# Optimization experiments

Measured on AMD Instinct MI355X. Metric: run time of the kernel, lower is better.

## Reference

```python
import jax, jax.numpy as jnp
import numpy as np

N_NODES = 100000
N_EDGES = 1600000
D_IN = 128
D_OUT = 128


def setup_inputs() -> dict:
    key = jax.random.key(0)
    k1, k2, k3, k4, k5 = jax.random.split(key, 5)
    h = jax.random.normal(k1, (N_NODES, D_IN), dtype=jnp.float32)
    src = jax.random.randint(k2, (N_EDGES,), 0, N_NODES, dtype=jnp.int64)
    dst = jax.random.randint(k3, (N_EDGES,), 0, N_NODES, dtype=jnp.int64)
    W = jax.random.normal(k4, (2 * D_IN, D_OUT), dtype=jnp.float32) * (1.0 / np.sqrt(2 * D_IN))
    b = jax.random.normal(k5, (D_OUT,), dtype=jnp.float32) * 0.01
    return {"h": h, "src": src, "dst": dst, "W": W, "b": b}


def reference(h, src, dst, W, b):
    # copy_u + mean: scatter-mean of source features onto destination nodes
    msg_sum = jax.ops.segment_sum(h[src], dst, num_segments=N_NODES)  # [N, D_IN]
    deg = jax.ops.segment_sum(jnp.ones((src.shape[0],), h.dtype), dst, num_segments=N_NODES)  # [N]
    h_N = jnp.where(deg[:, None] > 0, msg_sum / jnp.maximum(deg, 1.0)[:, None], 0.0)
    h_total = jnp.concatenate([h, h_N], axis=1)  # [N, 2*D_IN]
    return h_total @ W + b
```

## Files before the change

### kernel.cpp

```cpp
#include <hip/hip_runtime.h>
#include <stdint.h>

#define N_NODES 100000
#define D 128
#define BN 64
#define NB ((N_NODES + BN - 1) / BN)
#define CAPN 64
#define HPAD 136

typedef short bf16x8 __attribute__((ext_vector_type(8)));
typedef float f32x4 __attribute__((ext_vector_type(4)));

__device__ __forceinline__ unsigned short f2bf(float f) {
    unsigned int x = __float_as_uint(f);
    unsigned int r = x + 0x7fffu + ((x >> 16) & 1u);
    return (unsigned short)(r >> 16);
}
__device__ __forceinline__ float blo(unsigned int u) { return __uint_as_float(u << 16); }
__device__ __forceinline__ float bhi(unsigned int u) { return __uint_as_float(u & 0xffff0000u); }

__global__ __launch_bounds__(256) void prep_k(
    const float* __restrict__ h, unsigned short* __restrict__ h_bf,
    const float* __restrict__ W, unsigned short* __restrict__ Wf,
    const int* __restrict__ src, const int* __restrict__ dst,
    int* __restrict__ cnt, unsigned int* __restrict__ pairs,
    int n_edges, int cblocks, int epb)
{
    int bid = blockIdx.x;
    int t = threadIdx.x;

    if (bid < cblocks) {
        size_t base = ((size_t)bid * 256 + t) * 4;
        float4 v = *(const float4*)(h + base);

        for (int i = t; i < epb; i += 256) {
            int e = bid * epb + i;
            if (e < n_edges) {
                int d = dst[e];
                int slot = atomicAdd(&cnt[d], 1);
                if (slot < CAPN)
                    pairs[(size_t)d * CAPN + slot] = (unsigned int)src[e];
            }
        }

        ushort4 o;
        o.x = f2bf(v.x); o.y = f2bf(v.y); o.z = f2bf(v.z); o.w = f2bf(v.w);
        *(ushort4*)(h_bf + base) = o;
    } else {
        int gid = (bid - cblocks) * 256 + t;
        if (gid < 64 * 64) {
            int f = gid >> 6, l = gid & 63;
            int kt = f >> 3, ct = f & 7;
            int n = ct * 16 + (l & 15);
            int kb = kt * 32 + (l >> 4) * 8;
            #pragma unroll
            for (int j = 0; j < 8; ++j)
                Wf[(size_t)f * 512 + l * 8 + j] = f2bf(W[(size_t)(kb + j) * D + n]);
        }
    }
}

__global__ __launch_bounds__(512, 8) void aggemm_k(
    const unsigned short* __restrict__ h_bf, const unsigned int* __restrict__ pairs,
    const int* __restrict__ cnt_g, const unsigned short* __restrict__ Wf,
    const float* __restrict__ bias, float* __restrict__ out)
{
    __shared__ unsigned short hNs[BN][HPAD];

    int t = threadIdx.x;
    int b = blockIdx.x;
    int wv = t >> 6, l = t & 63;
    int q = l >> 4, lq = l & 15;
    int nbase = b * BN;

    #pragma unroll
    for (int p = 0; p < 2; ++p) {
        int nl = p * 32 + wv * 4 + q;
        int n = nbase + nl;
        int dg = 0;
        if (n < N_NODES) { dg = cnt_g[n]; if (dg > CAPN) dg = CAPN; }
        const unsigned int* ps = pairs + (size_t)(n < N_NODES ? n : 0) * CAPN;
        float a0 = 0.f, a1 = 0.f, a2 = 0.f, a3 = 0.f;
        float a4 = 0.f, a5 = 0.f, a6 = 0.f, a7 = 0.f;
        int i = 0;
        for (; i + 4 <= dg; i += 4) {
            uint4 s4 = *(const uint4*)(ps + i);
            uint4 u0 = *(const uint4*)(h_bf + (size_t)s4.x * D + lq * 8);
            uint4 u1 = *(const uint4*)(h_bf + (size_t)s4.y * D + lq * 8);
            uint4 u2 = *(const uint4*)(h_bf + (size_t)s4.z * D + lq * 8);
            uint4 u3 = *(const uint4*)(h_bf + (size_t)s4.w * D + lq * 8);
            a0 += (blo(u0.x) + blo(u1.x)) + (blo(u2.x) + blo(u3.x));
            a1 += (bhi(u0.x) + bhi(u1.x)) + (bhi(u2.x) + bhi(u3.x));
            a2 += (blo(u0.y) + blo(u1.y)) + (blo(u2.y) + blo(u3.y));
            a3 += (bhi(u0.y) + bhi(u1.y)) + (bhi(u2.y) + bhi(u3.y));
            a4 += (blo(u0.z) + blo(u1.z)) + (blo(u2.z) + blo(u3.z));
            a5 += (bhi(u0.z) + bhi(u1.z)) + (bhi(u2.z) + bhi(u3.z));
            a6 += (blo(u0.w) + blo(u1.w)) + (blo(u2.w) + blo(u3.w));
            a7 += (bhi(u0.w) + bhi(u1.w)) + (bhi(u2.w) + bhi(u3.w));
        }
        for (; i < dg; ++i) {
            uint4 u = *(const uint4*)(h_bf + (size_t)ps[i] * D + lq * 8);
            a0 += blo(u.x); a1 += bhi(u.x);
            a2 += blo(u.y); a3 += bhi(u.y);
            a4 += blo(u.z); a5 += bhi(u.z);
            a6 += blo(u.w); a7 += bhi(u.w);
        }
        float invd = dg > 0 ? 1.0f / (float)dg : 0.f;
        uint4 o;
        o.x = ((unsigned int)f2bf(a1 * invd) << 16) | f2bf(a0 * invd);
        o.y = ((unsigned int)f2bf(a3 * invd) << 16) | f2bf(a2 * invd);
        o.z = ((unsigned int)f2bf(a5 * invd) << 16) | f2bf(a4 * invd);
        o.w = ((unsigned int)f2bf(a7 * invd) << 16) | f2bf(a6 * invd);
        *(uint4*)(&hNs[nl][lq * 8]) = o;
    }
    __syncthreads();

    int rt = wv >> 1, ch = wv & 1;
    int lrow = l & 15, lqd = l >> 4;
    int lr = rt * 16 + lrow;
    int r0 = nbase + lr; if (r0 > N_NODES - 1) r0 = N_NODES - 1;

    f32x4 acc[4];
    #pragma unroll
    for (int c = 0; c < 4; ++c) acc[c] = (f32x4){0.f, 0.f, 0.f, 0.f};

    const unsigned short* wf_lane = Wf + l * 8;

    #pragma unroll
    for (int kt = 0; kt < 8; ++kt) {
        int ko = (kt & 3) * 32 + lqd * 8;
        bf16x8 a;
        if (kt < 4)
            a = *(const bf16x8*)(h_bf + (size_t)r0 * D + ko);
        else
            a = *(const bf16x8*)(&hNs[lr][ko]);
        #pragma unroll
        for (int c = 0; c < 4; ++c) {
            int ct = ch * 4 + c;
            bf16x8 bfr = *(const bf16x8*)(wf_lane + (size_t)(kt * 8 + ct) * 512);
            acc[c] = __builtin_amdgcn_mfma_f32_16x16x32_bf16(a, bfr, acc[c], 0, 0, 0);
        }
    }

    int col = l & 15, qd = l >> 4;
    #pragma unroll
    for (int c = 0; c < 4; ++c) {
        int ct = ch * 4 + c;
        float bv = bias[ct * 16 + col];
        #pragma unroll
        for (int r = 0; r < 4; ++r) {
            int row = nbase + rt * 16 + qd * 4 + r;
            if (row < N_NODES)
                out[(size_t)row * D + ct * 16 + col] = acc[c][r] + bv;
        }
    }
}


extern "C" void kernel_launch(void* const* d_in, const int* in_sizes, int n_in,
                              void* d_out, int out_size, void* d_ws, size_t ws_size,
                              hipStream_t stream) {
    const float* h  = (const float*)d_in[0];
    const int* src  = (const int*)d_in[1];
    const int* dst  = (const int*)d_in[2];
    const float* W  = (const float*)d_in[3];
    const float* b  = (const float*)d_in[4];
    float* out      = (float*)d_out;
    int n_edges = in_sizes[1];

    char* ws = (char*)d_ws;
    unsigned short* h_bf  = (unsigned short*)ws;
    unsigned int* pairs   = (unsigned int*)(h_bf + (size_t)N_NODES * D);
    unsigned short* Wf    = (unsigned short*)(pairs + (size_t)N_NODES * CAPN);
    int* cnt              = (int*)(Wf + 64 * 512);

    hipMemsetAsync(cnt, 0, N_NODES * sizeof(int), stream);

    int cblocks = (int)(((size_t)N_NODES * D / 4 + 255) / 256);
    int epb = (n_edges + cblocks - 1) / cblocks;
    hipLaunchKernelGGL(prep_k, dim3(cblocks + 16), dim3(256), 0, stream,
                       h, h_bf, W, Wf, src, dst, cnt, pairs, n_edges, cblocks, epb);

    hipLaunchKernelGGL(aggemm_k, dim3(NB), dim3(512), 0, stream,
                       h_bf, pairs, cnt, Wf, b, out);
}
```

Baseline: 265.1 us.

## Bucket edges per 64-node block with shared-histogram partition and in-block counting sort

Replaces per-destination global atomics and fixed 64-slot adjacency lists with a two-level partition. Each block builds a shared-memory histogram over 64-node buckets and reserves a range with one global atomic per bucket. The aggregation kernel then counting-sorts its bucket's packed (src, local dst) pairs in LDS. This removes heavy global atomic contention and the mostly empty padded adjacency storage. In exchange it adds large shared arrays per block (lowering occupancy), an extra in-block sort with several barriers, and a bucket cap of 1536 edges that could drop edges on skewed inputs.

```diff
diff --git a/kernel.cpp b/kernel.cpp
--- a/kernel.cpp
+++ b/kernel.cpp
@@ -5,7 +5,8 @@
 #define D 128
 #define BN 64
 #define NB ((N_NODES + BN - 1) / BN)
-#define CAPN 64
+#define EPB 4096
+#define CAP 1536
 #define HPAD 136
 
 typedef short bf16x8 __attribute__((ext_vector_type(8)));
@@ -24,30 +25,38 @@
     const float* __restrict__ W, unsigned short* __restrict__ Wf,
     const int* __restrict__ src, const int* __restrict__ dst,
     int* __restrict__ cnt, unsigned int* __restrict__ pairs,
-    int n_edges, int cblocks, int epb)
+    int n_edges, int partb)
 {
+    __shared__ int hist[NB];
+    __shared__ int lc[NB];
+
     int bid = blockIdx.x;
     int t = threadIdx.x;
 
-    if (bid < cblocks) {
-        size_t base = ((size_t)bid * 256 + t) * 4;
-        float4 v = *(const float4*)(h + base);
-
-        for (int i = t; i < epb; i += 256) {
-            int e = bid * epb + i;
-            if (e < n_edges) {
-                int d = dst[e];
-                int slot = atomicAdd(&cnt[d], 1);
-                if (slot < CAPN)
-                    pairs[(size_t)d * CAPN + slot] = (unsigned int)src[e];
-            }
-        }
-
-        ushort4 o;
-        o.x = f2bf(v.x); o.y = f2bf(v.y); o.z = f2bf(v.z); o.w = f2bf(v.w);
-        *(ushort4*)(h_bf + base) = o;
-    } else {
-        int gid = (bid - cblocks) * 256 + t;
+    if (bid < partb) {
+        for (int i = t; i < NB; i += 256) { hist[i] = 0; lc[i] = 0; }
+        __syncthreads();
+        int base = bid * EPB;
+        int lim = n_edges - base; if (lim > EPB) lim = EPB; if (lim < 0) lim = 0;
+        for (int i = t; i < lim; i += 256)
+            atomicAdd(&hist[dst[base + i] >> 6], 1);
+        __syncthreads();
+        for (int i = t; i < NB; i += 256) {
+            int c = hist[i];
+            hist[i] = c ? atomicAdd(&cnt[i], c) : 0;
+        }
+        __syncthreads();
+        for (int i = t; i < lim; i += 256) {
+            int e = base + i;
+            int d = dst[e], b = d >> 6;
+            int slot = atomicAdd(&lc[b], 1);
+            int off = hist[b] + slot;
+            if (off < CAP)
+                pairs[(size_t)b * CAP + off] =
+                    (unsigned int)src[e] | ((unsigned int)(d & 63) << 17);
+        }
+    } else if (bid < partb + 16) {
+        int gid = (bid - partb) * 256 + t;
         if (gid < 64 * 64) {
             int f = gid >> 6, l = gid & 63;
             int kt = f >> 3, ct = f & 7;
@@ -57,6 +66,14 @@
             for (int j = 0; j < 8; ++j)
                 Wf[(size_t)f * 512 + l * 8 + j] = f2bf(W[(size_t)(kb + j) * D + n]);
         }
+    } else {
+        size_t base = ((size_t)(bid - partb - 16) * 256 + t) * 4;
+        if (base < (size_t)N_NODES * D) {
+            float4 v = *(const float4*)(h + base);
+            ushort4 o;
+            o.x = f2bf(v.x); o.y = f2bf(v.y); o.z = f2bf(v.z); o.w = f2bf(v.w);
+            *(ushort4*)(h_bf + base) = o;
+        }
     }
 }
 
@@ -65,30 +82,70 @@
     const int* __restrict__ cnt_g, const unsigned short* __restrict__ Wf,
     const float* __restrict__ bias, float* __restrict__ out)
 {
+    __shared__ unsigned int lp[CAP];
+    __shared__ unsigned int srt[CAP];
+    __shared__ int counts[BN];
+    __shared__ int startp[BN];
+    __shared__ int cursor[BN];
     __shared__ unsigned short hNs[BN][HPAD];
 
     int t = threadIdx.x;
     int b = blockIdx.x;
     int wv = t >> 6, l = t & 63;
+    size_t e0 = (size_t)b * CAP;
+    int cnt = cnt_g[b];
+    if (cnt > CAP) cnt = CAP;
+
+    if (t < BN) counts[t] = 0;
+    __syncthreads();
+
+    for (int i = t; i < cnt; i += 512) {
+        unsigned int p = pairs[e0 + i];
+        lp[i] = p;
+        atomicAdd(&counts[p >> 17], 1);
+    }
+    __syncthreads();
+
+    if (t < BN) startp[t] = counts[t];
+    __syncthreads();
+    #pragma unroll
+    for (int off = 1; off < BN; off <<= 1) {
+        int v = 0;
+        if (t < BN && t >= off) v = startp[t - off];
+        __syncthreads();
+        if (t < BN) startp[t] += v;
+        __syncthreads();
+    }
+    if (t < BN) {
+        int ex = startp[t] - counts[t];
+        startp[t] = ex;
+        cursor[t] = ex;
+    }
+    __syncthreads();
+
+    for (int i = t; i < cnt; i += 512) {
+        unsigned int p = lp[i];
+        int s = atomicAdd(&cursor[p >> 17], 1);
+        srt[s] = p & 0x1FFFFu;
+    }
+    __syncthreads();
+
     int q = l >> 4, lq = l & 15;
     int nbase = b * BN;
-
-    #pragma unroll
-    for (int p = 0; p < 2; ++p) {
-        int nl = p * 32 + wv * 4 + q;
-        int n = nbase + nl;
-        int dg = 0;
-        if (n < N_NODES) { dg = cnt_g[n]; if (dg > CAPN) dg = CAPN; }
-        const unsigned int* ps = pairs + (size_t)(n < N_NODES ? n : 0) * CAPN;
+    #pragma unroll
+    for (int p2 = 0; p2 < 2; ++p2) {
+        int nl = p2 * 32 + wv * 4 + q;
+        int dg = counts[nl], s0 = startp[nl];
         float a0 = 0.f, a1 = 0.f, a2 = 0.f, a3 = 0.f;
         float a4 = 0.f, a5 = 0.f, a6 = 0.f, a7 = 0.f;
         int i = 0;
         for (; i + 4 <= dg; i += 4) {
-            uint4 s4 = *(const uint4*)(ps + i);
-            uint4 u0 = *(const uint4*)(h_bf + (size_t)s4.x * D + lq * 8);
-            uint4 u1 = *(const uint4*)(h_bf + (size_t)s4.y * D + lq * 8);
-            uint4 u2 = *(const uint4*)(h_bf + (size_t)s4.z * D + lq * 8);
-            uint4 u3 = *(const uint4*)(h_bf + (size_t)s4.w * D + lq * 8);
+            int s0i = srt[s0 + i],     s1i = srt[s0 + i + 1];
+            int s2i = srt[s0 + i + 2], s3i = srt[s0 + i + 3];
+            uint4 u0 = *(const uint4*)(h_bf + (size_t)s0i * D + lq * 8);
+            uint4 u1 = *(const uint4*)(h_bf + (size_t)s1i * D + lq * 8);
+            uint4 u2 = *(const uint4*)(h_bf + (size_t)s2i * D + lq * 8);
+            uint4 u3 = *(const uint4*)(h_bf + (size_t)s3i * D + lq * 8);
             a0 += (blo(u0.x) + blo(u1.x)) + (blo(u2.x) + blo(u3.x));
             a1 += (bhi(u0.x) + bhi(u1.x)) + (bhi(u2.x) + bhi(u3.x));
             a2 += (blo(u0.y) + blo(u1.y)) + (blo(u2.y) + blo(u3.y));
@@ -99,7 +156,7 @@
             a7 += (bhi(u0.w) + bhi(u1.w)) + (bhi(u2.w) + bhi(u3.w));
         }
         for (; i < dg; ++i) {
-            uint4 u = *(const uint4*)(h_bf + (size_t)ps[i] * D + lq * 8);
+            uint4 u = *(const uint4*)(h_bf + (size_t)srt[s0 + i] * D + lq * 8);
             a0 += blo(u.x); a1 += bhi(u.x);
             a2 += blo(u.y); a3 += bhi(u.y);
             a4 += blo(u.z); a5 += bhi(u.z);
@@ -171,15 +228,15 @@
     char* ws = (char*)d_ws;
     unsigned short* h_bf  = (unsigned short*)ws;
     unsigned int* pairs   = (unsigned int*)(h_bf + (size_t)N_NODES * D);
-    unsigned short* Wf    = (unsigned short*)(pairs + (size_t)N_NODES * CAPN);
+    unsigned short* Wf    = (unsigned short*)(pairs + (size_t)NB * CAP);
     int* cnt              = (int*)(Wf + 64 * 512);
 
-    hipMemsetAsync(cnt, 0, N_NODES * sizeof(int), stream);
-
+    hipMemsetAsync(cnt, 0, NB * sizeof(int), stream);
+
+    int partb = (n_edges + EPB - 1) / EPB;
     int cblocks = (int)(((size_t)N_NODES * D / 4 + 255) / 256);
-    int epb = (n_edges + cblocks - 1) / cblocks;
-    hipLaunchKernelGGL(prep_k, dim3(cblocks + 16), dim3(256), 0, stream,
-                       h, h_bf, W, Wf, src, dst, cnt, pairs, n_edges, cblocks, epb);
+    hipLaunchKernelGGL(prep_k, dim3(partb + 16 + cblocks), dim3(256), 0, stream,
+                       h, h_bf, W, Wf, src, dst, cnt, pairs, n_edges, partb);
 
     hipLaunchKernelGGL(aggemm_k, dim3(NB), dim3(512), 0, stream,
                        h_bf, pairs, cnt, Wf, b, out);
```

Result: faster. 227.8 us (-14.1%).
